# Optimization experiments

Hardware: AMD Instinct MI355X
Metric: run time of the kernel (lower is better)

## Reference

```python
import jax, jax.numpy as jnp
import numpy as np

T, S, W, D, C, K = 16, 16, 10, 512, 64, 512  # tasks, shots, ways, z_dim, n_concept, triplets/group


def setup_inputs() -> dict:
    key = jax.random.key(0)
    ks = jax.random.split(key, 12)
    sc = 0.02
    inp = {
        "input_data": jax.random.normal(ks[0], (T, S, W, D), dtype=jnp.float32),
        "triplet_idx": jax.random.randint(ks[1], (T, W, 3, K), 0, S * W, dtype=jnp.int64),
        # proj_inner: Linear(3D -> 2D), ReLU, Linear(2D -> D)
        "W1": jax.random.normal(ks[2], (3 * D, 2 * D), dtype=jnp.float32) * sc,
        "b1": jnp.zeros((2 * D,), dtype=jnp.float32),
        "W2": jax.random.normal(ks[3], (2 * D, D), dtype=jnp.float32) * sc,
        "b2": jnp.zeros((D,), dtype=jnp.float32),
        # proj_outer: Linear(D -> 2D), ReLU, Linear(2D -> D)
        "W3": jax.random.normal(ks[4], (D, 2 * D), dtype=jnp.float32) * sc,
        "b3": jnp.zeros((2 * D,), dtype=jnp.float32),
        "W4": jax.random.normal(ks[5], (2 * D, D), dtype=jnp.float32) * sc,
        "b4": jnp.zeros((D,), dtype=jnp.float32),
        # cls: Linear(D -> C)
        "Wc": jax.random.normal(ks[6], (D, C), dtype=jnp.float32) * sc,
        "bc": jnp.zeros((C,), dtype=jnp.float32),
    }
    return inp


def reference(input_data, triplet_idx, W1, b1, W2, b2, W3, b3, W4, b4, Wc, bc):
    t, s, w, d = input_data.shape
    x = input_data.reshape(t, s * w, d)                     # [T, N, D], N = shot*way
    # gather triplet embeddings: [T, W, 3, K, D]
    emb = x[jnp.arange(t)[:, None, None, None], triplet_idx]
    # permute([1,0,2]).reshape(-1, 3*dim): [T, W, K, 3*D]
    trip = jnp.swapaxes(emb, 2, 3).reshape(t, w, -1, 3 * d)
    # proj_inner MLP then sum over triplets
    h = jax.nn.relu(trip @ W1 + b1) @ W2 + b2               # [T, W, K, D]
    g = jnp.sum(h, axis=2)                                  # [T, W, D]
    # proj_outer MLP -> cls -> softmax
    o = jax.nn.relu(g @ W3 + b3) @ W4 + b4                  # [T, W, D]
    score = o @ Wc + bc                                     # [T, W, C]
    return jax.nn.softmax(score, axis=-1)
```

## Files before the change

### kernel.cpp

```cpp
#include <hip/hip_runtime.h>
#include <hip/hip_bf16.h>

#define T_  16
#define W_  10
#define D_  512
#define SW_ 160
#define N1_ 1024
#define KT_ 512

typedef __bf16 bf16x8 __attribute__((ext_vector_type(8)));
typedef float  f32x4  __attribute__((ext_vector_type(4)));

__device__ __forceinline__ void async16(const void* g, void* l) {
  __builtin_amdgcn_global_load_lds(
      (__attribute__((address_space(1))) void*)(g),
      (__attribute__((address_space(3))) void*)(l), 16, 0, 0);
}

__device__ __forceinline__ float lo16(unsigned v) { return __uint_as_float(v << 16); }
__device__ __forceinline__ float hi16(unsigned v) { return __uint_as_float(v & 0xffff0000u); }

__global__ __launch_bounds__(256) void cast_x(const float* __restrict__ xin,
                                              __hip_bfloat16* __restrict__ xbf) {
  int i = blockIdx.x * 256 + threadIdx.x;
  xbf[i] = __float2bfloat16(xin[i]);
}

__global__ __launch_bounds__(256) void transpose_w1(const float* __restrict__ W1,
                                                    __hip_bfloat16* __restrict__ w1t) {
  __shared__ float tile[32 * 33];
  int k0 = blockIdx.y * 32, n0 = blockIdx.x * 32;
  int c = threadIdx.x & 31, r0 = threadIdx.x >> 5;
#pragma unroll
  for (int i = 0; i < 4; ++i) {
    int r = r0 + i * 8;
    tile[r * 33 + c] = W1[(size_t)(k0 + r) * N1_ + n0 + c];
  }
  __syncthreads();
#pragma unroll
  for (int i = 0; i < 4; ++i) {
    int r = r0 + i * 8;
    w1t[(size_t)(n0 + r) * 1536 + k0 + c] = __float2bfloat16(tile[c * 33 + r]);
  }
}

__global__ __launch_bounds__(256) void transpose4(
    const float* __restrict__ W2, const float* __restrict__ W3,
    const float* __restrict__ W4, const float* __restrict__ Wc,
    __hip_bfloat16* __restrict__ W2t, __hip_bfloat16* __restrict__ W3t,
    __hip_bfloat16* __restrict__ W4t, __hip_bfloat16* __restrict__ Wct)
{
  const float* src; __hip_bfloat16* dst; int R, C;
  switch (blockIdx.z) {
    case 0:  src = W2; dst = W2t; R = 1024; C = 512;  break;
    case 1:  src = W3; dst = W3t; R = 512;  C = 1024; break;
    case 2:  src = W4; dst = W4t; R = 1024; C = 512;  break;
    default: src = Wc; dst = Wct; R = 512;  C = 64;   break;
  }
  int r0 = blockIdx.y * 32, c0 = blockIdx.x * 32;
  if (r0 >= R || c0 >= C) return;
  __shared__ float tile[32 * 33];
  int c = threadIdx.x & 31, rr = threadIdx.x >> 5;
#pragma unroll
  for (int i = 0; i < 4; ++i) {
    int r = rr + i * 8;
    tile[r * 33 + c] = src[(size_t)(r0 + r) * C + c0 + c];
  }
  __syncthreads();
#pragma unroll
  for (int i = 0; i < 4; ++i) {
    int r = rr + i * 8;
    dst[(size_t)(c0 + r) * R + r0 + c] = __float2bfloat16(tile[c * 33 + r]);
  }
}

__global__ __launch_bounds__(256) void group_kernel(
    const __hip_bfloat16* __restrict__ xbf,
    const __hip_bfloat16* __restrict__ w1t,
    const int* __restrict__ tidx,
    const float* __restrict__ b1,
    __hip_bfloat16* __restrict__ Hsb)
{
  __shared__ __align__(16) char smem[43008];
  char* Abuf  = smem;
  char* Bbuf  = smem + 20480;
  char* Ptile = smem;
  int*  idx_s = (int*)(smem + 34560);
  float* red  = (float*)(smem + 40704);

  const int tid = threadIdx.x;
  const int bx  = blockIdx.x;
  const int t   = bx >> 5;
  const int nt  = bx & 31;
  const int n0  = nt << 5;

  const int ln = tid & 63, wv = tid >> 6;
  const int wr = wv >> 1, wc = wv & 1;
  const int col16 = ln & 15, quad = ln >> 4;

  const __hip_bfloat16* xt = xbf + (size_t)t * (SW_ * D_);

  int aoff[5], lofA[5];
#pragma unroll
  for (int s = 0; s < 5; ++s) {
    int i = s * 256 + tid, r = i >> 3, q = i & 7;
    aoff[s] = r * 512 + ((q ^ (r & 7)) << 3);
    lofA[s] = i << 4;
  }
  int boff[3], lofB[3];
#pragma unroll
  for (int s = 0; s < 3; ++s) {
    int i = s * 256 + tid, r = i >> 3, q = i & 7;
    int nc = r & 31, j = r >> 5;
    boff[s] = (n0 + nc) * 1536 + j * 512 + ((q ^ (r & 7)) << 3);
    lofB[s] = i << 4;
  }

  f32x4 acc[5][3];
#pragma unroll
  for (int a = 0; a < 5; ++a)
#pragma unroll
    for (int b = 0; b < 3; ++b)
      acc[a][b] = (f32x4){0.f, 0.f, 0.f, 0.f};

#pragma unroll 1
  for (int kk = 0; kk < 512; kk += 64) {
    __syncthreads();
#pragma unroll
    for (int s = 0; s < 5; ++s) async16(xt + aoff[s] + kk, Abuf + lofA[s]);
#pragma unroll
    for (int s = 0; s < 3; ++s) async16(w1t + boff[s] + kk, Bbuf + lofB[s]);
    __syncthreads();

#pragma unroll
    for (int ks = 0; ks < 2; ++ks) {
      const int qq = (ks << 2) + quad;
      bf16x8 af[5], bfr[3];
#pragma unroll
      for (int a = 0; a < 5; ++a) {
        int rm = wr * 80 + a * 16 + col16;
        af[a] = *(const bf16x8*)(Abuf + rm * 128 + ((qq ^ (rm & 7)) << 4));
      }
#pragma unroll
      for (int b = 0; b < 3; ++b) {
        int rn = wc * 48 + b * 16 + col16;
        bfr[b] = *(const bf16x8*)(Bbuf + rn * 128 + ((qq ^ (rn & 7)) << 4));
      }
#pragma unroll
      for (int a = 0; a < 5; ++a)
#pragma unroll
        for (int b = 0; b < 3; ++b)
          acc[a][b] = __builtin_amdgcn_mfma_f32_16x16x32_bf16(af[a], bfr[b], acc[a][b], 0, 0, 0);
    }
  }

  __syncthreads();

#pragma unroll
  for (int a = 0; a < 5; ++a)
#pragma unroll
    for (int b = 0; b < 3; ++b) {
      int c = wc * 48 + b * 16 + col16;
      int j = c >> 5, nc = c & 31;
      int mb = wr * 80 + a * 16 + quad * 4;
#pragma unroll
      for (int r = 0; r < 4; ++r)
        *(__hip_bfloat16*)(Ptile + (j * 160 + mb + r) * 72 + nc * 2) =
            __float2bfloat16(acc[a][b][r]);
    }

  const int nq = tid & 7;
  const int kq = tid >> 3;
  const float4 bias4 = *(const float4*)(b1 + n0 + (nq << 2));

#pragma unroll 1
  for (int w = 0; w < 10; ++w) {
    __syncthreads();
    {
      const int* src = tidx + (size_t)(t * 10 + w) * 1536;
      async16(src + (tid << 2), (char*)idx_s + (tid << 4));
      if (tid < 128) async16(src + 1024 + (tid << 2), (char*)idx_s + 4096 + (tid << 4));
    }
    __syncthreads();

    f32x4 a4 = (f32x4){0.f, 0.f, 0.f, 0.f};
#pragma unroll
    for (int u = 0; u < 4; ++u) {
      const int kb = (kq << 4) + (u << 2);
      int4 i0 = *(const int4*)(idx_s + kb);
      int4 i1 = *(const int4*)(idx_s + 512 + kb);
      int4 i2 = *(const int4*)(idx_s + 1024 + kb);
#define STEP(IA, IB, IC)                                                          \
      {                                                                           \
        uint2 p0 = *(const uint2*)(Ptile + (IA) * 72 + (nq << 3));                \
        uint2 p1 = *(const uint2*)(Ptile + 11520 + (IB) * 72 + (nq << 3));        \
        uint2 p2 = *(const uint2*)(Ptile + 23040 + (IC) * 72 + (nq << 3));        \
        a4.x += fmaxf(lo16(p0.x) + lo16(p1.x) + lo16(p2.x) + bias4.x, 0.f);       \
        a4.y += fmaxf(hi16(p0.x) + hi16(p1.x) + hi16(p2.x) + bias4.y, 0.f);       \
        a4.z += fmaxf(lo16(p0.y) + lo16(p1.y) + lo16(p2.y) + bias4.z, 0.f);       \
        a4.w += fmaxf(hi16(p0.y) + hi16(p1.y) + hi16(p2.y) + bias4.w, 0.f);       \
      }
      STEP(i0.x, i1.x, i2.x)
      STEP(i0.y, i1.y, i2.y)
      STEP(i0.z, i1.z, i2.z)
      STEP(i0.w, i1.w, i2.w)
#undef STEP
    }

#pragma unroll
    for (int off = 8; off <= 32; off <<= 1) {
      a4.x += __shfl_xor(a4.x, off);
      a4.y += __shfl_xor(a4.y, off);
      a4.z += __shfl_xor(a4.z, off);
      a4.w += __shfl_xor(a4.w, off);
    }
    if ((ln >> 3) == 0)
      *(f32x4*)(red + wv * 32 + (nq << 2)) = a4;
    __syncthreads();
    if (tid < 32) {
      float s = red[tid] + red[32 + tid] + red[64 + tid] + red[96 + tid];
      Hsb[(size_t)(t * 10 + w) * N1_ + n0 + tid] = __float2bfloat16(s);
    }
  }
}

__global__ __launch_bounds__(256) void tail_gemm(
    const __hip_bfloat16* __restrict__ A,
    const __hip_bfloat16* __restrict__ Bt,
    const float* __restrict__ bias, float bscale, int relu, int K, int N,
    __hip_bfloat16* __restrict__ out)
{
  __shared__ __align__(16) char Abuf[20480];
  __shared__ __align__(16) char Bbuf[16384];
  const int tid = threadIdx.x;
  const int n0 = blockIdx.x << 6;
  const int m0 = blockIdx.y * 80;
  const int ln = tid & 63, wv = tid >> 6;
  const int col16 = ln & 15, quad = ln >> 4;

  f32x4 acc[5];
#pragma unroll
  for (int a = 0; a < 5; ++a) acc[a] = (f32x4){0.f, 0.f, 0.f, 0.f};

#pragma unroll 1
  for (int kk = 0; kk < K; kk += 128) {
    __syncthreads();
#pragma unroll
    for (int p = 0; p < 5; ++p) {
      int i = p * 256 + tid, r = i >> 4, q = i & 15;
      async16(A + (size_t)(m0 + r) * K + kk + ((q ^ (r & 7)) << 3), Abuf + (i << 4));
    }
#pragma unroll
    for (int p = 0; p < 4; ++p) {
      int i = p * 256 + tid, r = i >> 4, q = i & 15;
      async16(Bt + (size_t)(n0 + r) * K + kk + ((q ^ (r & 7)) << 3), Bbuf + (i << 4));
    }
    __syncthreads();

#pragma unroll
    for (int ks = 0; ks < 4; ++ks) {
      const int qq = (ks << 2) + quad;
      const int rn = (wv << 4) + col16;
      bf16x8 bf = *(const bf16x8*)(Bbuf + rn * 256 + ((qq ^ (rn & 7)) << 4));
#pragma unroll
      for (int a = 0; a < 5; ++a) {
        int rm = (a << 4) + col16;
        bf16x8 af = *(const bf16x8*)(Abuf + rm * 256 + ((qq ^ (rm & 7)) << 4));
        acc[a] = __builtin_amdgcn_mfma_f32_16x16x32_bf16(af, bf, acc[a], 0, 0, 0);
      }
    }
  }

  const int n = n0 + (wv << 4) + col16;
  const float bb = bias[n] * bscale;
#pragma unroll
  for (int a = 0; a < 5; ++a)
#pragma unroll
    for (int r = 0; r < 4; ++r) {
      float v = acc[a][r] + bb;
      if (relu) v = fmaxf(v, 0.f);
      out[(size_t)(m0 + (a << 4) + (quad << 2) + r) * N + n] = __float2bfloat16(v);
    }
}

__global__ __launch_bounds__(256) void head_gemm(
    const __hip_bfloat16* __restrict__ A,
    const __hip_bfloat16* __restrict__ Bt,
    const float* __restrict__ bc,
    float* __restrict__ out)
{
  __shared__ __align__(16) char Abuf[20480];
  __shared__ __align__(16) char Bbuf[16384];
  __shared__ float sc[80 * 64];
  __shared__ float rs[80];
  const int tid = threadIdx.x;
  const int m0 = blockIdx.x * 80;
  const int ln = tid & 63, wv = tid >> 6;
  const int col16 = ln & 15, quad = ln >> 4;

  f32x4 acc[5];
#pragma unroll
  for (int a = 0; a < 5; ++a) acc[a] = (f32x4){0.f, 0.f, 0.f, 0.f};

#pragma unroll 1
  for (int kk = 0; kk < 512; kk += 128) {
    __syncthreads();
#pragma unroll
    for (int p = 0; p < 5; ++p) {
      int i = p * 256 + tid, r = i >> 4, q = i & 15;
      async16(A + (size_t)(m0 + r) * 512 + kk + ((q ^ (r & 7)) << 3), Abuf + (i << 4));
    }
#pragma unroll
    for (int p = 0; p < 4; ++p) {
      int i = p * 256 + tid, r = i >> 4, q = i & 15;
      async16(Bt + (size_t)r * 512 + kk + ((q ^ (r & 7)) << 3), Bbuf + (i << 4));
    }
    __syncthreads();

#pragma unroll
    for (int ks = 0; ks < 4; ++ks) {
      const int qq = (ks << 2) + quad;
      const int rn = (wv << 4) + col16;
      bf16x8 bf = *(const bf16x8*)(Bbuf + rn * 256 + ((qq ^ (rn & 7)) << 4));
#pragma unroll
      for (int a = 0; a < 5; ++a) {
        int rm = (a << 4) + col16;
        bf16x8 af = *(const bf16x8*)(Abuf + rm * 256 + ((qq ^ (rm & 7)) << 4));
        acc[a] = __builtin_amdgcn_mfma_f32_16x16x32_bf16(af, bf, acc[a], 0, 0, 0);
      }
    }
  }

  const int n = (wv << 4) + col16;
  const float bb = bc[n];
#pragma unroll
  for (int a = 0; a < 5; ++a)
#pragma unroll
    for (int r = 0; r < 4; ++r)
      sc[((a << 4) + (quad << 2) + r) * 64 + n] = acc[a][r] + bb;
  __syncthreads();

  if (tid < 80) {
    float m = -1e30f;
    for (int c = 0; c < 64; ++c) m = fmaxf(m, sc[tid * 64 + c]);
    float s = 0.f;
    for (int c = 0; c < 64; ++c) {
      float e = expf(sc[tid * 64 + c] - m);
      sc[tid * 64 + c] = e;
      s += e;
    }
    rs[tid] = 1.f / s;
  }
  __syncthreads();
#pragma unroll
  for (int p = 0; p < 20; ++p) {
    int f = p * 256 + tid, r = f >> 6, c = f & 63;
    out[(size_t)(m0 + r) * 64 + c] = sc[f] * rs[r];
  }
}

extern "C" void kernel_launch(void* const* d_in, const int* in_sizes, int n_in,
                              void* d_out, int out_size, void* d_ws, size_t ws_size,
                              hipStream_t stream) {
  const float* x_in = (const float*)d_in[0];
  const int*   tidx = (const int*)d_in[1];
  const float* W1 = (const float*)d_in[2];
  const float* b1 = (const float*)d_in[3];
  const float* W2 = (const float*)d_in[4];
  const float* b2 = (const float*)d_in[5];
  const float* W3 = (const float*)d_in[6];
  const float* b3 = (const float*)d_in[7];
  const float* W4 = (const float*)d_in[8];
  const float* b4 = (const float*)d_in[9];
  const float* Wc = (const float*)d_in[10];
  const float* bc = (const float*)d_in[11];
  float* out = (float*)d_out;
  (void)in_sizes; (void)n_in; (void)out_size; (void)ws_size;

  char* ws = (char*)d_ws;
  __hip_bfloat16* xbf = (__hip_bfloat16*)(ws + 0);
  __hip_bfloat16* w1t = (__hip_bfloat16*)(ws + 2621440);
  __hip_bfloat16* W2t = (__hip_bfloat16*)(ws + 0);
  __hip_bfloat16* W3t = (__hip_bfloat16*)(ws + 1048576);
  __hip_bfloat16* W4t = (__hip_bfloat16*)(ws + 2097152);
  __hip_bfloat16* Wct = (__hip_bfloat16*)(ws + 3145728);
  __hip_bfloat16* Hsb = (__hip_bfloat16*)(ws + 5767168);
  __hip_bfloat16* gb  = (__hip_bfloat16*)(ws + 6094848);
  __hip_bfloat16* ub  = (__hip_bfloat16*)(ws + 6258688);
  __hip_bfloat16* ob  = (__hip_bfloat16*)(ws + 6586368);

  cast_x<<<5120, 256, 0, stream>>>(x_in, xbf);
  transpose_w1<<<dim3(32, 48), 256, 0, stream>>>(W1, w1t);

  group_kernel<<<512, 256, 0, stream>>>(xbf, w1t, tidx, b1, Hsb);

  transpose4<<<dim3(32, 32, 4), 256, 0, stream>>>(W2, W3, W4, Wc, W2t, W3t, W4t, Wct);

  tail_gemm<<<dim3(8, 2), 256, 0, stream>>>(Hsb, W2t, b2, (float)KT_, 0, 1024, 512, gb);
  tail_gemm<<<dim3(16, 2), 256, 0, stream>>>(gb, W3t, b3, 1.f, 1, 512, 1024, ub);
  tail_gemm<<<dim3(8, 2), 256, 0, stream>>>(ub, W4t, b4, 1.f, 0, 1024, 512, ob);
  head_gemm<<<2, 256, 0, stream>>>(ob, Wct, bc, out);
}
```

Measured before the change: 165.1 us.

## Fold linear layer pairs into precomputed weights and merge prep kernels

Exploits the lack of a nonlinearity between W2 and W3, and between W4 and Wc, to precompute the products W2·W3 and W4·Wc, with folded biases, inside a widened group kernel. The fused weights are stored as bf16 hi/lo split pairs, so the later GEMMs run over a doubled K to keep precision. This cuts the tail from four dependent GEMM launches to two. All cast and transpose prep is merged into one launch. In exchange, the weight-product GEMMs are recomputed on every call, the tail GEMMs do twice the K work, and LDS use per block goes up.

After: 186.2 us. +12.7%, slower.

```diff
diff --git a/kernel.cpp b/kernel.cpp
--- a/kernel.cpp
+++ b/kernel.cpp
@@ -20,83 +20,160 @@
 __device__ __forceinline__ float lo16(unsigned v) { return __uint_as_float(v << 16); }
 __device__ __forceinline__ float hi16(unsigned v) { return __uint_as_float(v & 0xffff0000u); }
 
-__global__ __launch_bounds__(256) void cast_x(const float* __restrict__ xin,
-                                              __hip_bfloat16* __restrict__ xbf) {
-  int i = blockIdx.x * 256 + threadIdx.x;
-  xbf[i] = __float2bfloat16(xin[i]);
-}
-
-__global__ __launch_bounds__(256) void transpose_w1(const float* __restrict__ W1,
-                                                    __hip_bfloat16* __restrict__ w1t) {
-  __shared__ float tile[32 * 33];
-  int k0 = blockIdx.y * 32, n0 = blockIdx.x * 32;
-  int c = threadIdx.x & 31, r0 = threadIdx.x >> 5;
-#pragma unroll
-  for (int i = 0; i < 4; ++i) {
-    int r = r0 + i * 8;
-    tile[r * 33 + c] = W1[(size_t)(k0 + r) * N1_ + n0 + c];
-  }
-  __syncthreads();
-#pragma unroll
-  for (int i = 0; i < 4; ++i) {
-    int r = r0 + i * 8;
-    w1t[(size_t)(n0 + r) * 1536 + k0 + c] = __float2bfloat16(tile[c * 33 + r]);
-  }
-}
-
-__global__ __launch_bounds__(256) void transpose4(
+__global__ __launch_bounds__(256) void prep_all(
+    const float* __restrict__ x_in, const float* __restrict__ W1,
     const float* __restrict__ W2, const float* __restrict__ W3,
     const float* __restrict__ W4, const float* __restrict__ Wc,
-    __hip_bfloat16* __restrict__ W2t, __hip_bfloat16* __restrict__ W3t,
-    __hip_bfloat16* __restrict__ W4t, __hip_bfloat16* __restrict__ Wct)
+    const float* __restrict__ b2, const float* __restrict__ b3,
+    const float* __restrict__ b4, const float* __restrict__ bc,
+    __hip_bfloat16* __restrict__ xbf, __hip_bfloat16* __restrict__ w1t,
+    __hip_bfloat16* __restrict__ w2b, __hip_bfloat16* __restrict__ w3t,
+    __hip_bfloat16* __restrict__ w4b, __hip_bfloat16* __restrict__ wct,
+    float* __restrict__ b23, float* __restrict__ bc4)
 {
-  const float* src; __hip_bfloat16* dst; int R, C;
-  switch (blockIdx.z) {
-    case 0:  src = W2; dst = W2t; R = 1024; C = 512;  break;
-    case 1:  src = W3; dst = W3t; R = 512;  C = 1024; break;
-    case 2:  src = W4; dst = W4t; R = 1024; C = 512;  break;
-    default: src = Wc; dst = Wct; R = 512;  C = 64;   break;
-  }
-  int r0 = blockIdx.y * 32, c0 = blockIdx.x * 32;
-  if (r0 >= R || c0 >= C) return;
   __shared__ float tile[32 * 33];
-  int c = threadIdx.x & 31, rr = threadIdx.x >> 5;
-#pragma unroll
-  for (int i = 0; i < 4; ++i) {
-    int r = rr + i * 8;
-    tile[r * 33 + c] = src[(size_t)(r0 + r) * C + c0 + c];
-  }
-  __syncthreads();
-#pragma unroll
-  for (int i = 0; i < 4; ++i) {
-    int r = rr + i * 8;
-    dst[(size_t)(c0 + r) * R + r0 + c] = __float2bfloat16(tile[c * 33 + r]);
-  }
-}
-
-__global__ __launch_bounds__(256) void group_kernel(
+  const int b = blockIdx.x, tid = threadIdx.x;
+
+  auto cast4 = [&](const float* src, __hip_bfloat16* dst, int base) {
+    int i = (base + tid) << 2;
+    float4 v = *(const float4*)(src + i);
+    __align__(8) __hip_bfloat16 o4[4];
+    o4[0] = __float2bfloat16(v.x); o4[1] = __float2bfloat16(v.y);
+    o4[2] = __float2bfloat16(v.z); o4[3] = __float2bfloat16(v.w);
+    *(uint2*)(dst + i) = *(const uint2*)o4;
+  };
+  auto tr32 = [&](const float* src, __hip_bfloat16* dst, int R, int C, int rt, int ct) {
+    int r0 = rt << 5, c0 = ct << 5;
+    int c = tid & 31, rr = tid >> 5;
+#pragma unroll
+    for (int i = 0; i < 4; ++i) {
+      int r = rr + i * 8;
+      tile[r * 33 + c] = src[(size_t)(r0 + r) * C + c0 + c];
+    }
+    __syncthreads();
+#pragma unroll
+    for (int i = 0; i < 4; ++i) {
+      int r = rr + i * 8;
+      dst[(size_t)(c0 + r) * R + r0 + c] = __float2bfloat16(tile[c * 33 + r]);
+    }
+  };
+
+  if (b < 1280) {
+    cast4(x_in, xbf, b * 256);
+  } else if (b < 2816) {
+    int q = b - 1280; tr32(W1, w1t, 1536, 1024, q >> 5, q & 31);
+  } else if (b < 3328) {
+    cast4(W2, w2b, (b - 2816) * 256);
+  } else if (b < 3840) {
+    int q = b - 3328; tr32(W3, w3t, 512, 1024, q >> 5, q & 31);
+  } else if (b < 4352) {
+    cast4(W4, w4b, (b - 3840) * 256);
+  } else if (b < 4384) {
+    int q = b - 4352; tr32(Wc, wct, 512, 64, q >> 1, q & 1);
+  } else if (b < 4388) {
+    int c = (b - 4384) * 256 + tid;
+    float s = 0.f;
+#pragma unroll 8
+    for (int j = 0; j < 512; ++j) s += b2[j] * W3[(size_t)j * 1024 + c];
+    b23[c] = 512.f * s + b3[c];
+  } else {
+    if (tid < 64) {
+      float s = 0.f;
+#pragma unroll 8
+      for (int j = 0; j < 512; ++j) s += b4[j] * Wc[(size_t)j * 64 + tid];
+      bc4[tid] = s + bc[tid];
+    }
+  }
+}
+
+__global__ __launch_bounds__(256) void group_wgemm(
     const __hip_bfloat16* __restrict__ xbf,
     const __hip_bfloat16* __restrict__ w1t,
     const int* __restrict__ tidx,
     const float* __restrict__ b1,
-    __hip_bfloat16* __restrict__ Hsb)
+    __hip_bfloat16* __restrict__ Hsb,
+    const __hip_bfloat16* __restrict__ w3t,
+    const __hip_bfloat16* __restrict__ w2b,
+    const __hip_bfloat16* __restrict__ wct,
+    const __hip_bfloat16* __restrict__ w4b,
+    __hip_bfloat16* __restrict__ w23t,
+    __hip_bfloat16* __restrict__ w4ct)
 {
   __shared__ __align__(16) char smem[43008];
+  const int bx = blockIdx.x;
+  const int tid = threadIdx.x;
+  const int ln = tid & 63, wv = tid >> 6;
+  const int col16 = ln & 15, quad = ln >> 4;
+
+  if (bx >= 512) {
+    const int b = bx - 512;
+    const __hip_bfloat16 *A, *Bt;
+    __hip_bfloat16* out;
+    int m0, n0;
+    if (b < 256) { A = w3t; Bt = w2b; out = w23t; m0 = (b >> 4) << 6; n0 = (b & 15) << 6; }
+    else         { A = wct; Bt = w4b; out = w4ct; m0 = 0;             n0 = (b - 256) << 6; }
+    char* Abuf = smem;
+    char* Bbuf = smem + 16384;
+
+    f32x4 acc[4];
+#pragma unroll
+    for (int a = 0; a < 4; ++a) acc[a] = (f32x4){0.f, 0.f, 0.f, 0.f};
+
+#pragma unroll 1
+    for (int kk = 0; kk < 512; kk += 128) {
+      __syncthreads();
+#pragma unroll
+      for (int p = 0; p < 4; ++p) {
+        int i = p * 256 + tid, r = i >> 4, q = i & 15;
+        async16(A + (size_t)(m0 + r) * 512 + kk + ((q ^ (r & 7)) << 3), Abuf + (i << 4));
+      }
+#pragma unroll
+      for (int p = 0; p < 4; ++p) {
+        int i = p * 256 + tid, r = i >> 4, q = i & 15;
+        async16(Bt + (size_t)(n0 + r) * 512 + kk + ((q ^ (r & 7)) << 3), Bbuf + (i << 4));
+      }
+      __syncthreads();
+
+#pragma unroll
+      for (int ks = 0; ks < 4; ++ks) {
+        const int qq = (ks << 2) + quad;
+        const int rn = (wv << 4) + col16;
+        bf16x8 bfm = *(const bf16x8*)(Bbuf + rn * 256 + ((qq ^ (rn & 7)) << 4));
+#pragma unroll
+        for (int a = 0; a < 4; ++a) {
+          int rm = (a << 4) + col16;
+          bf16x8 af = *(const bf16x8*)(Abuf + rm * 256 + ((qq ^ (rm & 7)) << 4));
+          acc[a] = __builtin_amdgcn_mfma_f32_16x16x32_bf16(af, bfm, acc[a], 0, 0, 0);
+        }
+      }
+    }
+
+    const int n = n0 + (wv << 4) + col16;
+#pragma unroll
+    for (int a = 0; a < 4; ++a)
+#pragma unroll
+      for (int r = 0; r < 4; ++r) {
+        float v = acc[a][r];
+        __hip_bfloat16 h = __float2bfloat16(v);
+        float lres = v - __bfloat162float(h);
+        size_t row = m0 + (a << 4) + (quad << 2) + r;
+        out[row * 2048 + n] = h;
+        out[row * 2048 + 1024 + n] = __float2bfloat16(lres);
+      }
+    return;
+  }
+
   char* Abuf  = smem;
   char* Bbuf  = smem + 20480;
   char* Ptile = smem;
   int*  idx_s = (int*)(smem + 34560);
   float* red  = (float*)(smem + 40704);
 
-  const int tid = threadIdx.x;
-  const int bx  = blockIdx.x;
   const int t   = bx >> 5;
   const int nt  = bx & 31;
   const int n0  = nt << 5;
 
-  const int ln = tid & 63, wv = tid >> 6;
   const int wr = wv >> 1, wc = wv & 1;
-  const int col16 = ln & 15, quad = ln >> 4;
 
   const __hip_bfloat16* xt = xbf + (size_t)t * (SW_ * D_);
 
@@ -224,14 +301,14 @@
   }
 }
 
-__global__ __launch_bounds__(256) void tail_gemm(
+__global__ __launch_bounds__(256) void mid_gemm(
     const __hip_bfloat16* __restrict__ A,
     const __hip_bfloat16* __restrict__ Bt,
-    const float* __restrict__ bias, float bscale, int relu, int K, int N,
+    const float* __restrict__ bias,
     __hip_bfloat16* __restrict__ out)
 {
-  __shared__ __align__(16) char Abuf[20480];
-  __shared__ __align__(16) char Bbuf[16384];
+  __shared__ __align__(16) char Abuf[40960];
+  __shared__ __align__(16) char Bbuf[32768];
   const int tid = threadIdx.x;
   const int n0 = blockIdx.x << 6;
   const int m0 = blockIdx.y * 80;
@@ -243,54 +320,54 @@
   for (int a = 0; a < 5; ++a) acc[a] = (f32x4){0.f, 0.f, 0.f, 0.f};
 
 #pragma unroll 1
-  for (int kk = 0; kk < K; kk += 128) {
-    __syncthreads();
-#pragma unroll
-    for (int p = 0; p < 5; ++p) {
-      int i = p * 256 + tid, r = i >> 4, q = i & 15;
-      async16(A + (size_t)(m0 + r) * K + kk + ((q ^ (r & 7)) << 3), Abuf + (i << 4));
-    }
-#pragma unroll
-    for (int p = 0; p < 4; ++p) {
-      int i = p * 256 + tid, r = i >> 4, q = i & 15;
-      async16(Bt + (size_t)(n0 + r) * K + kk + ((q ^ (r & 7)) << 3), Bbuf + (i << 4));
-    }
-    __syncthreads();
-
-#pragma unroll
-    for (int ks = 0; ks < 4; ++ks) {
+  for (int kk = 0; kk < 2048; kk += 256) {
+    const int ka = kk & 1023;
+    __syncthreads();
+#pragma unroll
+    for (int p = 0; p < 10; ++p) {
+      int i = p * 256 + tid, r = i >> 5, q = i & 31;
+      async16(A + (size_t)(m0 + r) * 1024 + ka + ((q ^ (r & 7)) << 3), Abuf + (i << 4));
+    }
+#pragma unroll
+    for (int p = 0; p < 8; ++p) {
+      int i = p * 256 + tid, r = i >> 5, q = i & 31;
+      async16(Bt + (size_t)(n0 + r) * 2048 + kk + ((q ^ (r & 7)) << 3), Bbuf + (i << 4));
+    }
+    __syncthreads();
+
+#pragma unroll
+    for (int ks = 0; ks < 8; ++ks) {
       const int qq = (ks << 2) + quad;
       const int rn = (wv << 4) + col16;
-      bf16x8 bf = *(const bf16x8*)(Bbuf + rn * 256 + ((qq ^ (rn & 7)) << 4));
+      bf16x8 bfm = *(const bf16x8*)(Bbuf + rn * 512 + ((qq ^ (rn & 7)) << 4));
 #pragma unroll
       for (int a = 0; a < 5; ++a) {
         int rm = (a << 4) + col16;
-        bf16x8 af = *(const bf16x8*)(Abuf + rm * 256 + ((qq ^ (rm & 7)) << 4));
-        acc[a] = __builtin_amdgcn_mfma_f32_16x16x32_bf16(af, bf, acc[a], 0, 0, 0);
+        bf16x8 af = *(const bf16x8*)(Abuf + rm * 512 + ((qq ^ (rm & 7)) << 4));
+        acc[a] = __builtin_amdgcn_mfma_f32_16x16x32_bf16(af, bfm, acc[a], 0, 0, 0);
       }
     }
   }
 
   const int n = n0 + (wv << 4) + col16;
-  const float bb = bias[n] * bscale;
+  const float bb = bias[n];
 #pragma unroll
   for (int a = 0; a < 5; ++a)
 #pragma unroll
     for (int r = 0; r < 4; ++r) {
-      float v = acc[a][r] + bb;
-      if (relu) v = fmaxf(v, 0.f);
-      out[(size_t)(m0 + (a << 4) + (quad << 2) + r) * N + n] = __float2bfloat16(v);
-    }
-}
-
-__global__ __launch_bounds__(256) void head_gemm(
+      float v = fmaxf(acc[a][r] + bb, 0.f);
+      out[(size_t)(m0 + (a << 4) + (quad << 2) + r) * 1024 + n] = __float2bfloat16(v);
+    }
+}
+
+__global__ __launch_bounds__(256) void head_gemm2(
     const __hip_bfloat16* __restrict__ A,
     const __hip_bfloat16* __restrict__ Bt,
-    const float* __restrict__ bc,
+    const float* __restrict__ bc4,
     float* __restrict__ out)
 {
-  __shared__ __align__(16) char Abuf[20480];
-  __shared__ __align__(16) char Bbuf[16384];
+  __shared__ __align__(16) char Abuf[40960];
+  __shared__ __align__(16) char Bbuf[32768];
   __shared__ float sc[80 * 64];
   __shared__ float rs[80];
   const int tid = threadIdx.x;
@@ -303,36 +380,37 @@
   for (int a = 0; a < 5; ++a) acc[a] = (f32x4){0.f, 0.f, 0.f, 0.f};
 
 #pragma unroll 1
-  for (int kk = 0; kk < 512; kk += 128) {
-    __syncthreads();
-#pragma unroll
-    for (int p = 0; p < 5; ++p) {
-      int i = p * 256 + tid, r = i >> 4, q = i & 15;
-      async16(A + (size_t)(m0 + r) * 512 + kk + ((q ^ (r & 7)) << 3), Abuf + (i << 4));
-    }
-#pragma unroll
-    for (int p = 0; p < 4; ++p) {
-      int i = p * 256 + tid, r = i >> 4, q = i & 15;
-      async16(Bt + (size_t)r * 512 + kk + ((q ^ (r & 7)) << 3), Bbuf + (i << 4));
-    }
-    __syncthreads();
-
-#pragma unroll
-    for (int ks = 0; ks < 4; ++ks) {
+  for (int kk = 0; kk < 2048; kk += 256) {
+    const int ka = kk & 1023;
+    __syncthreads();
+#pragma unroll
+    for (int p = 0; p < 10; ++p) {
+      int i = p * 256 + tid, r = i >> 5, q = i & 31;
+      async16(A + (size_t)(m0 + r) * 1024 + ka + ((q ^ (r & 7)) << 3), Abuf + (i << 4));
+    }
+#pragma unroll
+    for (int p = 0; p < 8; ++p) {
+      int i = p * 256 + tid, r = i >> 5, q = i & 31;
+      async16(Bt + (size_t)r * 2048 + kk + ((q ^ (r & 7)) << 3), Bbuf + (i << 4));
+    }
+    __syncthreads();
+
+#pragma unroll
+    for (int ks = 0; ks < 8; ++ks) {
       const int qq = (ks << 2) + quad;
       const int rn = (wv << 4) + col16;
-      bf16x8 bf = *(const bf16x8*)(Bbuf + rn * 256 + ((qq ^ (rn & 7)) << 4));
+      bf16x8 bfm = *(const bf16x8*)(Bbuf + rn * 512 + ((qq ^ (rn & 7)) << 4));
 #pragma unroll
       for (int a = 0; a < 5; ++a) {
         int rm = (a << 4) + col16;
-        bf16x8 af = *(const bf16x8*)(Abuf + rm * 256 + ((qq ^ (rm & 7)) << 4));
-        acc[a] = __builtin_amdgcn_mfma_f32_16x16x32_bf16(af, bf, acc[a], 0, 0, 0);
+        bf16x8 af = *(const bf16x8*)(Abuf + rm * 512 + ((qq ^ (rm & 7)) << 4));
+        acc[a] = __builtin_amdgcn_mfma_f32_16x16x32_bf16(af, bfm, acc[a], 0, 0, 0);
       }
     }
   }
 
   const int n = (wv << 4) + col16;
-  const float bb = bc[n];
+  const float bb = bc4[n];
 #pragma unroll
   for (int a = 0; a < 5; ++a)
 #pragma unroll
@@ -378,26 +456,26 @@
   (void)in_sizes; (void)n_in; (void)out_size; (void)ws_size;
 
   char* ws = (char*)d_ws;
-  __hip_bfloat16* xbf = (__hip_bfloat16*)(ws + 0);
-  __hip_bfloat16* w1t = (__hip_bfloat16*)(ws + 2621440);
-  __hip_bfloat16* W2t = (__hip_bfloat16*)(ws + 0);
-  __hip_bfloat16* W3t = (__hip_bfloat16*)(ws + 1048576);
-  __hip_bfloat16* W4t = (__hip_bfloat16*)(ws + 2097152);
-  __hip_bfloat16* Wct = (__hip_bfloat16*)(ws + 3145728);
-  __hip_bfloat16* Hsb = (__hip_bfloat16*)(ws + 5767168);
-  __hip_bfloat16* gb  = (__hip_bfloat16*)(ws + 6094848);
-  __hip_bfloat16* ub  = (__hip_bfloat16*)(ws + 6258688);
-  __hip_bfloat16* ob  = (__hip_bfloat16*)(ws + 6586368);
-
-  cast_x<<<5120, 256, 0, stream>>>(x_in, xbf);
-  transpose_w1<<<dim3(32, 48), 256, 0, stream>>>(W1, w1t);
-
-  group_kernel<<<512, 256, 0, stream>>>(xbf, w1t, tidx, b1, Hsb);
-
-  transpose4<<<dim3(32, 32, 4), 256, 0, stream>>>(W2, W3, W4, Wc, W2t, W3t, W4t, Wct);
-
-  tail_gemm<<<dim3(8, 2), 256, 0, stream>>>(Hsb, W2t, b2, (float)KT_, 0, 1024, 512, gb);
-  tail_gemm<<<dim3(16, 2), 256, 0, stream>>>(gb, W3t, b3, 1.f, 1, 512, 1024, ub);
-  tail_gemm<<<dim3(8, 2), 256, 0, stream>>>(ub, W4t, b4, 1.f, 0, 1024, 512, ob);
-  head_gemm<<<2, 256, 0, stream>>>(ob, Wct, bc, out);
-}
+  __hip_bfloat16* xbf  = (__hip_bfloat16*)(ws + 0);
+  __hip_bfloat16* w1t  = (__hip_bfloat16*)(ws + 2621440);
+  __hip_bfloat16* w2b  = (__hip_bfloat16*)(ws + 5767168);
+  __hip_bfloat16* w3t  = (__hip_bfloat16*)(ws + 6815744);
+  __hip_bfloat16* w4b  = (__hip_bfloat16*)(ws + 7864320);
+  __hip_bfloat16* wct  = (__hip_bfloat16*)(ws + 8912896);
+  float*          b23  = (float*)         (ws + 8978432);
+  float*          bc4  = (float*)         (ws + 8982528);
+  __hip_bfloat16* Hsb  = (__hip_bfloat16*)(ws + 8982784);
+  __hip_bfloat16* w23t = (__hip_bfloat16*)(ws + 9310464);
+  __hip_bfloat16* w4ct = (__hip_bfloat16*)(ws + 13504768);
+  __hip_bfloat16* ub   = (__hip_bfloat16*)(ws + 13766912);
+
+  prep_all<<<4389, 256, 0, stream>>>(x_in, W1, W2, W3, W4, Wc, b2, b3, b4, bc,
+                                     xbf, w1t, w2b, w3t, w4b, wct, b23, bc4);
+
+  group_wgemm<<<784, 256, 0, stream>>>(xbf, w1t, tidx, b1, Hsb,
+                                       w3t, w2b, wct, w4b, w23t, w4ct);
+
+  mid_gemm<<<dim3(16, 2), 256, 0, stream>>>(Hsb, w23t, b23, ub);
+
+  head_gemm2<<<2, 256, 0, stream>>>(ub, w4ct, bc4, out);
+}
```
